# Kernel tuning notes

Hardware: AMD Instinct MI355X
Metric: run time of the kernel (lower is better)

Reference implementation:

```python
import jax, jax.numpy as jnp
import numpy as np

B, D = 8192, 768
TOP_K = 5


def setup_inputs() -> dict:
    key = jax.random.key(0)
    ks = jax.random.split(key, 12)
    # xavier_uniform bound for (D, D)
    bg = float(np.sqrt(6.0 / (D + D)))
    def xav(k, fan_in, fan_out):
        b = float(np.sqrt(6.0 / (fan_in + fan_out)))
        return jax.random.uniform(k, (fan_in, fan_out), jnp.float32, -b, b)
    return {
        "X": jax.random.normal(ks[0], (B, D), jnp.float32),
        "A_ecfp": jax.random.uniform(ks[1], (B, B), jnp.float32),
        "W_g": jax.random.uniform(ks[2], (D, D), jnp.float32, -bg, bg),
        "raw_alpha": jnp.zeros((), jnp.float32),
        "W_gcn": xav(ks[3], D, D),
        "b_gcn": jnp.zeros((D,), jnp.float32),
        "W1": xav(ks[4], D, 512),
        "b1": jnp.zeros((512,), jnp.float32),
        "W2": xav(ks[5], 512, 256),
        "b2": jnp.zeros((256,), jnp.float32),
        "W3": xav(ks[6], 256, 1),
        "b3": jnp.zeros((1,), jnp.float32),
    }


def _forward(X, A_ecfp, W_g, raw_alpha, W_gcn, b_gcn, W1, b1, W2, b2, W3, b3):
    n = X.shape[0]
    # learned similarity, blended with ECFP prior
    S = jax.nn.relu((X @ W_g) @ X.T)                    # (B, B)
    alpha = jax.nn.sigmoid(raw_alpha)
    A = alpha * A_ecfp + (1.0 - alpha) * S
    # top-k sparsification per row, symmetrized (OR)
    k = min(TOP_K, n - 1)
    _, top_idx = jax.lax.top_k(A, k)                    # (B, k)
    rows = jnp.arange(n)[:, None]
    mask = jnp.zeros_like(A).at[rows, top_idx].set(1.0)
    mask = ((mask + mask.T) > 0).astype(A.dtype)
    A = A * mask
    # zero diagonal, then add self-loops (diagonal becomes 1)
    diag = jnp.eye(n, dtype=A.dtype)
    A = A * (1.0 - diag) + diag
    # degree normalization D^-1 A
    D_inv = 1.0 / jnp.clip(A.sum(-1, keepdims=True), 1e-8)
    A_norm = A * D_inv
    # single GCN layer (exact erf GELU, matching torch default)
    H = jax.nn.gelu(A_norm @ X @ W_gcn + b_gcn, approximate=False)
    # MLP head (dropout is identity in eval)
    h = jax.nn.gelu(H @ W1 + b1, approximate=False)
    h = jax.nn.gelu(h @ W2 + b2, approximate=False)
    return h @ W3 + b3                                  # (B, 1)


def reference(X, A_ecfp, W_g, raw_alpha, W_gcn, b_gcn, W1, b1, W2, b2, W3, b3):
    return _forward(X, A_ecfp, W_g, raw_alpha, W_gcn, b_gcn, W1, b1, W2, b2, W3, b3)
```

## Files before the change

kernel.cpp:

```cpp
#include <hip/hip_runtime.h>
#include <math.h>


typedef __attribute__((ext_vector_type(8))) short short8v;
typedef __attribute__((ext_vector_type(4))) float f32x4;

__device__ __forceinline__ unsigned short f2bf(float f) {
  unsigned u = __float_as_uint(f);
  u += 0x7fffu + ((u >> 16) & 1u);
  return (unsigned short)(u >> 16);
}
__device__ __forceinline__ float bf2f(unsigned short h) {
  return __uint_as_float(((unsigned)h) << 16);
}
__device__ __forceinline__ float gelu_f(float x) {
  return 0.5f * x * (1.f + erff(x * 0.7071067811865475f));
}
__device__ __forceinline__ void gload16(const void* g, void* l) {
  __builtin_amdgcn_global_load_lds(
      (const __attribute__((address_space(1))) unsigned int*)g,
      (__attribute__((address_space(3))) unsigned int*)l, 16, 0, 0);
}

template <int N>
__device__ __forceinline__ void insN(float v, int j, float (&lv)[N], int (&li)[N]) {
#pragma unroll
  for (int p = N - 1; p >= 1; --p) {
    bool shiftv = v > lv[p - 1];
    bool here = (v > lv[p]) && !shiftv;
    float nv = shiftv ? lv[p - 1] : (here ? v : lv[p]);
    int ni = shiftv ? li[p - 1] : (here ? j : li[p]);
    lv[p] = nv; li[p] = ni;
  }
  if (v > lv[0]) { lv[0] = v; li[0] = j; }
}

__global__ __launch_bounds__(256) void cvt_bf16(const float* __restrict__ in,
                                                unsigned short* __restrict__ out, int n4) {
  int t = blockIdx.x * 256 + threadIdx.x;
  if (t >= n4) return;
  float4 f = ((const float4*)in)[t];
  ushort4 r;
  r.x = f2bf(f.x); r.y = f2bf(f.y); r.z = f2bf(f.z); r.w = f2bf(f.w);
  ((ushort4*)out)[t] = r;
}

__global__ __launch_bounds__(256) void split2(const float* __restrict__ in,
                                              unsigned short* __restrict__ out,
                                              int K, int n4) {
  int t = blockIdx.x * 256 + threadIdx.x;
  if (t >= n4) return;
  int kq = K >> 2;
  int row = t / kq, c4 = t - row * kq;
  float4 f = ((const float4*)in)[t];
  ushort4 h, l;
  float x;
  x = f.x; h.x = f2bf(x); l.x = f2bf(x - bf2f(h.x));
  x = f.y; h.y = f2bf(x); l.y = f2bf(x - bf2f(h.y));
  x = f.z; h.z = f2bf(x); l.z = f2bf(x - bf2f(h.z));
  x = f.w; h.w = f2bf(x); l.w = f2bf(x - bf2f(h.w));
  *(ushort4*)(out + (size_t)row * 2 * K + c4 * 4) = h;
  *(ushort4*)(out + (size_t)row * 2 * K + K + c4 * 4) = l;
}

__global__ __launch_bounds__(256) void split_wt2(const float* __restrict__ W,
                                                 unsigned short* __restrict__ t2,
                                                 int K, int N) {
  __shared__ float tile[32][33];
  int kb = blockIdx.x * 32, nb = blockIdx.y * 32;
  int tx = threadIdx.x & 31, ty = threadIdx.x >> 5;
#pragma unroll
  for (int p = 0; p < 4; ++p)
    tile[ty + p * 8][tx] = W[(size_t)(kb + ty + p * 8) * N + nb + tx];
  __syncthreads();
#pragma unroll
  for (int p = 0; p < 4; ++p) {
    int n = ty + p * 8;
    float x = tile[tx][n];
    unsigned short h = f2bf(x);
    unsigned short l = f2bf(x - bf2f(h));
    t2[(size_t)(nb + n) * (2 * K) + kb + tx] = h;
    t2[(size_t)(nb + n) * (2 * K) + K + kb + tx] = l;
  }
}

__global__ __launch_bounds__(256) void sgemm_f32(const float* __restrict__ A,
                                                 const float* __restrict__ Bm,
                                                 float* __restrict__ C,
                                                 unsigned short* __restrict__ Cbf,
                                                 int N, int K) {
  __shared__ float As[16][68];
  __shared__ float Bs[16][132];
  const int r0 = blockIdx.x * 64, c0 = blockIdx.y * 128;
  const int tid = threadIdx.x;
  const int tr = tid >> 4, tc = tid & 15;
  float acc[4][8];
#pragma unroll
  for (int i = 0; i < 4; ++i)
#pragma unroll
    for (int j = 0; j < 8; ++j) acc[i][j] = 0.f;

  for (int k0 = 0; k0 < K; k0 += 16) {
    {
      int row = tid >> 2, kq = tid & 3;
      float4 a4 = *(const float4*)(A + (size_t)(r0 + row) * K + k0 + kq * 4);
      As[kq * 4 + 0][row] = a4.x; As[kq * 4 + 1][row] = a4.y;
      As[kq * 4 + 2][row] = a4.z; As[kq * 4 + 3][row] = a4.w;
#pragma unroll
      for (int s = 0; s < 2; ++s) {
        int ch = tid + s * 256;
        int kk = ch >> 5, nq = ch & 31;
        *(float4*)&Bs[kk][nq * 4] = *(const float4*)(Bm + (size_t)(k0 + kk) * N + c0 + nq * 4);
      }
    }
    __syncthreads();
#pragma unroll
    for (int k = 0; k < 16; ++k) {
      float a[4], b[8];
      *(float4*)&a[0] = *(const float4*)&As[k][tr * 4];
      *(float4*)&b[0] = *(const float4*)&Bs[k][tc * 8];
      *(float4*)&b[4] = *(const float4*)&Bs[k][tc * 8 + 4];
#pragma unroll
      for (int i = 0; i < 4; ++i)
#pragma unroll
        for (int j = 0; j < 8; ++j) acc[i][j] = fmaf(a[i], b[j], acc[i][j]);
    }
    __syncthreads();
  }
#pragma unroll
  for (int i = 0; i < 4; ++i) {
    int r = r0 + tr * 4 + i;
#pragma unroll
    for (int jq = 0; jq < 2; ++jq) {
      *(float4*)(C + (size_t)r * N + c0 + tc * 8 + jq * 4) = *(float4*)&acc[i][jq * 4];
      ushort4 hb;
      hb.x = f2bf(acc[i][jq * 4 + 0]); hb.y = f2bf(acc[i][jq * 4 + 1]);
      hb.z = f2bf(acc[i][jq * 4 + 2]); hb.w = f2bf(acc[i][jq * 4 + 3]);
      *(ushort4*)(Cbf + (size_t)r * N + c0 + tc * 8 + jq * 4) = hb;
    }
  }
}

template <int EPI>
__global__ __launch_bounds__(256) void gemm_bt(const unsigned short* __restrict__ A,
                                               const unsigned short* __restrict__ Bt,
                                               const float* __restrict__ bias,
                                               float* __restrict__ C, int N, int K) {
  __shared__ __align__(16) unsigned short As[128 * 64];
  __shared__ __align__(16) unsigned short Bs[128 * 64];
  const int r0 = blockIdx.x * 128, c0 = blockIdx.y * 128;
  const int tid = threadIdx.x, lane = tid & 63, w = tid >> 6;
  const int wr = w >> 1, wc = w & 1;
  f32x4 acc[4][4];
  const f32x4 z4 = {0.f, 0.f, 0.f, 0.f};
#pragma unroll
  for (int i = 0; i < 4; ++i)
#pragma unroll
    for (int j = 0; j < 4; ++j) acc[i][j] = z4;

  const int srow = w * 32 + (lane >> 3);
  const int ksl = (lane & 7) ^ (lane >> 3);
  const unsigned short* aSrc = A + (size_t)(r0 + srow) * K + ksl * 8;
  const unsigned short* bSrc = Bt + (size_t)(c0 + srow) * K + ksl * 8;
  const int rsw = (lane & 7);

  for (int k0 = 0; k0 < K; k0 += 64) {
#pragma unroll
    for (int t = 0; t < 4; ++t) {
      gload16(aSrc + k0 + (size_t)t * 8 * K, (char*)As + (w * 32 + t * 8) * 128);
      gload16(bSrc + k0 + (size_t)t * 8 * K, (char*)Bs + (w * 32 + t * 8) * 128);
    }
    __syncthreads();
#pragma unroll
    for (int ks = 0; ks < 2; ++ks) {
      short8v af[4], bf[4];
      const int slot = ((ks * 4 + (lane >> 4)) ^ rsw) << 4;
#pragma unroll
      for (int f = 0; f < 4; ++f) {
        af[f] = *(const short8v*)((const char*)As + (wr * 64 + f * 16 + (lane & 15)) * 128 + slot);
        bf[f] = *(const short8v*)((const char*)Bs + (wc * 64 + f * 16 + (lane & 15)) * 128 + slot);
      }
#pragma unroll
      for (int fi = 0; fi < 4; ++fi)
#pragma unroll
        for (int fj = 0; fj < 4; ++fj)
          acc[fi][fj] = __builtin_amdgcn_mfma_f32_16x16x32_bf16(af[fi], bf[fj], acc[fi][fj], 0, 0, 0);
    }
    __syncthreads();
  }
#pragma unroll
  for (int fi = 0; fi < 4; ++fi)
#pragma unroll
    for (int fj = 0; fj < 4; ++fj) {
      int col = c0 + wc * 64 + fj * 16 + (lane & 15);
      int rowb = r0 + wr * 64 + fi * 16 + (lane >> 4) * 4;
#pragma unroll
      for (int r = 0; r < 4; ++r) {
        size_t idx = (size_t)(rowb + r) * N + col;
        float x = acc[fi][fj][r];
        if constexpr (EPI) x = gelu_f(x + bias[col]);
        C[idx] = x;
      }
    }
}

__global__ __launch_bounds__(512, 4) void s_topk(const unsigned short* __restrict__ Gh,
                                                 const unsigned short* __restrict__ Xh,
                                                 float* __restrict__ pv, int* __restrict__ pix) {
  __shared__ __align__(16) unsigned short As[128 * 64];
  __shared__ __align__(16) unsigned short Bs[128 * 64];
  const int bid = blockIdx.x;
  const int r0 = (bid >> 3) * 128;
  const int chunk = bid & 7;
  const int tid = threadIdx.x, lane = tid & 63, w = tid >> 6;
  const int wr = w >> 2, wc = w & 3;
  float lv0[5], lv1[5]; int li0[5], li1[5];
#pragma unroll
  for (int q = 0; q < 5; ++q) {
    lv0[q] = -1e30f; li0[q] = 0; lv1[q] = -1e30f; li1[q] = 0;
  }

  const int strow = tid >> 3, sslot = tid & 7;
  const int ksl = sslot ^ (strow & 7);
  const unsigned short* bSrc = Gh + (size_t)(r0 + strow) * 768 + ksl * 8;
  char* aDst0 = (char*)As + strow * 128 + sslot * 16;
  char* bDst0 = (char*)Bs + strow * 128 + sslot * 16;
  const int rsw = lane & 7;

  for (int jt = 0; jt < 8; ++jt) {
    const int j0 = chunk * 1024 + jt * 128;
    const unsigned short* aSrc = Xh + (size_t)(j0 + strow) * 768 + ksl * 8;
    f32x4 acc[4][2];
    const f32x4 z4 = {0.f, 0.f, 0.f, 0.f};
#pragma unroll
    for (int i = 0; i < 4; ++i) {
      acc[i][0] = z4; acc[i][1] = z4;
    }

    for (int k0 = 0; k0 < 768; k0 += 64) {
      gload16(aSrc + k0, aDst0);
      gload16(aSrc + k0 + (size_t)64 * 768, aDst0 + 64 * 128);
      gload16(bSrc + k0, bDst0);
      gload16(bSrc + k0 + (size_t)64 * 768, bDst0 + 64 * 128);
      __syncthreads();
#pragma unroll
      for (int ks = 0; ks < 2; ++ks) {
        short8v aj[4], bi[2];
        const int slot = ((ks * 4 + (lane >> 4)) ^ rsw) << 4;
#pragma unroll
        for (int f = 0; f < 4; ++f)
          aj[f] = *(const short8v*)((const char*)As + (wr * 64 + f * 16 + (lane & 15)) * 128 + slot);
#pragma unroll
        for (int f = 0; f < 2; ++f)
          bi[f] = *(const short8v*)((const char*)Bs + (wc * 32 + f * 16 + (lane & 15)) * 128 + slot);
#pragma unroll
        for (int fi = 0; fi < 4; ++fi) {
          acc[fi][0] = __builtin_amdgcn_mfma_f32_16x16x32_bf16(aj[fi], bi[0], acc[fi][0], 0, 0, 0);
          acc[fi][1] = __builtin_amdgcn_mfma_f32_16x16x32_bf16(aj[fi], bi[1], acc[fi][1], 0, 0, 0);
        }
      }
      __syncthreads();
    }
    const int jb = j0 + wr * 64 + (lane >> 4) * 4;
#pragma unroll
    for (int fi = 0; fi < 4; ++fi)
#pragma unroll
      for (int r = 0; r < 4; ++r) {
        int jj = jb + fi * 16 + r;
        float v0 = acc[fi][0][r];
        if (v0 > lv0[4]) insN<5>(v0, jj, lv0, li0);
        float v1 = acc[fi][1][r];
        if (v1 > lv1[4]) insN<5>(v1, jj, lv1, li1);
      }
  }
  const int slotw = wr * 4 + (lane >> 4);
  const int ib0 = r0 + wc * 32 + (lane & 15);
  size_t base0 = (((size_t)ib0 * 8 + chunk) * 8 + slotw) * 5;
#pragma unroll
  for (int q = 0; q < 5; ++q) { pv[base0 + q] = lv0[q]; pix[base0 + q] = li0[q]; }
  size_t base1 = (((size_t)(ib0 + 16) * 8 + chunk) * 8 + slotw) * 5;
#pragma unroll
  for (int q = 0; q < 5; ++q) { pv[base1 + q] = lv1[q]; pix[base1 + q] = li1[q]; }
}

__global__ __launch_bounds__(256) void merge16(const float* __restrict__ pv,
                                               const int* __restrict__ pix,
                                               int* __restrict__ gidx) {
  int row = blockIdx.x * 256 + threadIdx.x;
  float lv[16]; int li[16];
#pragma unroll
  for (int q = 0; q < 16; ++q) { lv[q] = -1e30f; li[q] = 0; }
  for (int ch = 0; ch < 8; ++ch)
#pragma unroll
    for (int sl = 0; sl < 8; ++sl) {
      size_t base = (((size_t)row * 8 + ch) * 8 + sl) * 5;
#pragma unroll
      for (int q = 0; q < 5; ++q) {
        float v = pv[base + q];
        if (v > lv[15]) insN<16>(v, pix[base + q], lv, li);
      }
    }
#pragma unroll
  for (int q = 0; q < 16; ++q) gidx[row * 16 + q] = li[q];
}

__global__ __launch_bounds__(256) void refine5(const float* __restrict__ G,
                                               const float* __restrict__ X,
                                               const float* __restrict__ Ae,
                                               const int* __restrict__ gidx,
                                               const float* __restrict__ ralpha,
                                               int* __restrict__ t5i, float* __restrict__ t5v) {
  int i = blockIdx.x * 4 + (threadIdx.x >> 6);
  int lane = threadIdx.x & 63;
  int c = lane >> 2, s = lane & 3;
  float sa = 1.f / (1.f + expf(-ralpha[0]));
  int j = gidx[i * 16 + c];
  const float* g = G + (size_t)i * 768;
  const float* x = X + (size_t)j * 768;
  float a = 0.f;
#pragma unroll 8
  for (int t = 0; t < 192; ++t) a = fmaf(g[s + 4 * t], x[s + 4 * t], a);
  a += __shfl_xor(a, 1);
  a += __shfl_xor(a, 2);
  float v = sa * Ae[(size_t)i * 8192 + j] + (1.f - sa) * fmaxf(a, 0.f);
  float vs[16]; int js[16];
#pragma unroll
  for (int q = 0; q < 16; ++q) { vs[q] = __shfl(v, q * 4); js[q] = __shfl(j, q * 4); }
  if (lane == 0) {
    unsigned used = 0;
#pragma unroll
    for (int t = 0; t < 5; ++t) {
      float bv = -1e30f; int bj = 0; int bq = 0; bool any = false;
#pragma unroll
      for (int q = 0; q < 16; ++q) {
        bool ok = ((used >> q) & 1u) == 0u;
        bool better = ok && (!any || vs[q] > bv || (vs[q] == bv && js[q] < bj));
        bv = better ? vs[q] : bv; bj = better ? js[q] : bj; bq = better ? q : bq;
        any = any || better;
      }
      used |= (1u << bq);
      t5v[(size_t)i * 5 + t] = bv;
      t5i[(size_t)i * 5 + t] = bj;
    }
  }
}

__global__ void edge_deg(const int* __restrict__ t5i, int* __restrict__ deg) {
  int e = blockIdx.x * 256 + threadIdx.x;
  if (e >= 40960) return;
  int i = e / 5, t = e - i * 5;
  int j = t5i[i * 5 + t];
  if (j == i) return;
  bool rev = false;
#pragma unroll
  for (int u = 0; u < 5; ++u) rev = rev || (t5i[j * 5 + u] == i);
  if (!rev || i < j) { atomicAdd(&deg[i], 1); atomicAdd(&deg[j], 1); }
}

__global__ void scan8k(const int* __restrict__ deg, int* __restrict__ off) {
  __shared__ int sums[256];
  int tid = threadIdx.x;
  int base = tid * 32;
  int s = 0;
  for (int u = 0; u < 32; ++u) s += deg[base + u];
  sums[tid] = s;
  __syncthreads();
  for (int d = 1; d < 256; d <<= 1) {
    int v = (tid >= d) ? sums[tid - d] : 0;
    __syncthreads();
    sums[tid] += v;
    __syncthreads();
  }
  int run = tid ? sums[tid - 1] : 0;
  for (int u = 0; u < 32; ++u) { off[base + u] = run; run += deg[base + u]; }
  if (tid == 255) off[8192] = run;
}

__global__ __launch_bounds__(256) void edge_fill(const int* __restrict__ t5i,
                                                 const float* __restrict__ t5v,
                                                 const float* __restrict__ G,
                                                 const float* __restrict__ X,
                                                 const float* __restrict__ Ae,
                                                 const float* __restrict__ ralpha,
                                                 const int* __restrict__ off,
                                                 int* __restrict__ cursor,
                                                 int* __restrict__ ccol, float* __restrict__ cval) {
  int e = blockIdx.x * 4 + (threadIdx.x >> 6);
  if (e >= 40960) return;
  int lane = threadIdx.x & 63;
  int i = e / 5, t = e - i * 5;
  int j = t5i[i * 5 + t];
  if (j == i) return;
  int rev = -1;
#pragma unroll
  for (int u = 0; u < 5; ++u)
    if (t5i[j * 5 + u] == i) rev = u;
  if (!(rev < 0 || i < j)) return;
  float vji;
  if (rev >= 0) {
    vji = t5v[j * 5 + rev];
  } else {
    const float* g = G + (size_t)j * 768;
    const float* x = X + (size_t)i * 768;
    float a = 0.f;
#pragma unroll
    for (int u = 0; u < 12; ++u) a = fmaf(g[lane + 64 * u], x[lane + 64 * u], a);
#pragma unroll
    for (int d = 32; d; d >>= 1) a += __shfl_xor(a, d);
    float sa = 1.f / (1.f + expf(-ralpha[0]));
    vji = sa * Ae[(size_t)j * 8192 + i] + (1.f - sa) * fmaxf(a, 0.f);
  }
  if (lane == 0) {
    float vij = t5v[i * 5 + t];
    int p0 = off[i] + atomicAdd(&cursor[i], 1);
    ccol[p0] = j; cval[p0] = vij;
    int p1 = off[j] + atomicAdd(&cursor[j], 1);
    ccol[p1] = i; cval[p1] = vji;
  }
}

__global__ __launch_bounds__(256) void gather_gcn(const float* __restrict__ X,
                                                  const int* __restrict__ off,
                                                  const int* __restrict__ ccol,
                                                  const float* __restrict__ cval,
                                                  float* __restrict__ M) {
  __shared__ float red[256];
  __shared__ float sdinv;
  int i = blockIdx.x, tid = threadIdx.x;
  int s0 = off[i], cnt = off[i + 1] - s0;
  float s = 0.f;
  for (int e = tid; e < cnt; e += 256) s += cval[s0 + e];
  red[tid] = s;
  __syncthreads();
  for (int d = 128; d; d >>= 1) {
    if (tid < d) red[tid] += red[tid + d];
    __syncthreads();
  }
  if (tid == 0) sdinv = 1.f / fmaxf(1.f + red[0], 1e-8f);
  __syncthreads();
  float dinv = sdinv;
  const float* xi = X + (size_t)i * 768;
  float a0 = xi[tid], a1 = xi[tid + 256], a2 = xi[tid + 512];
  for (int e = 0; e < cnt; ++e) {
    float v = cval[s0 + e];
    const float* xr = X + (size_t)ccol[s0 + e] * 768;
    a0 = fmaf(v, xr[tid], a0);
    a1 = fmaf(v, xr[tid + 256], a1);
    a2 = fmaf(v, xr[tid + 512], a2);
  }
  float* mi = M + (size_t)i * 768;
  mi[tid] = a0 * dinv; mi[tid + 256] = a1 * dinv; mi[tid + 512] = a2 * dinv;
}

__global__ __launch_bounds__(256) void final_head(const float* __restrict__ h2,
                                                  const float* __restrict__ W3,
                                                  const float* __restrict__ b3,
                                                  float* __restrict__ out) {
  int i = blockIdx.x * 4 + (threadIdx.x >> 6);
  int lane = threadIdx.x & 63;
  const float* r = h2 + (size_t)i * 256;
  float s = r[lane] * W3[lane] + r[lane + 64] * W3[lane + 64] +
            r[lane + 128] * W3[lane + 128] + r[lane + 192] * W3[lane + 192];
#pragma unroll
  for (int d = 32; d; d >>= 1) s += __shfl_xor(s, d);
  if (lane == 0) out[i] = s + b3[0];
}

extern "C" void kernel_launch(void* const* d_in, const int* in_sizes, int n_in,
                              void* d_out, int out_size, void* d_ws, size_t ws_size,
                              hipStream_t stream) {
  const float* X   = (const float*)d_in[0];
  const float* Ae  = (const float*)d_in[1];
  const float* Wg  = (const float*)d_in[2];
  const float* ra  = (const float*)d_in[3];
  const float* Wgc = (const float*)d_in[4];
  const float* bgc = (const float*)d_in[5];
  const float* W1  = (const float*)d_in[6];
  const float* b1  = (const float*)d_in[7];
  const float* W2  = (const float*)d_in[8];
  const float* b2  = (const float*)d_in[9];
  const float* W3  = (const float*)d_in[10];
  const float* b3  = (const float*)d_in[11];
  float* out = (float*)d_out;

  char* w = (char*)d_ws;
  size_t off_ = 0;
  auto take = [&](size_t n) -> void* {
    void* p = w + off_;
    off_ += (n + 255) & ~(size_t)255;
    return p;
  };
  float* G            = (float*)take((size_t)8192 * 768 * 4);
  unsigned short* Xh  = (unsigned short*)take((size_t)8192 * 768 * 2);
  unsigned short* Gh  = (unsigned short*)take((size_t)8192 * 768 * 2);
  float* pv           = (float*)take((size_t)8192 * 320 * 4);
  int* pix            = (int*)take((size_t)8192 * 320 * 4);
  int* gidx           = (int*)take((size_t)8192 * 16 * 4);
  int* t5i            = (int*)take((size_t)8192 * 5 * 4);
  float* t5v          = (float*)take((size_t)8192 * 5 * 4);
  int* deg            = (int*)take((size_t)8192 * 4);
  int* offr           = (int*)take((size_t)8193 * 4);
  int* cur            = (int*)take((size_t)8192 * 4);
  int* ccol           = (int*)take((size_t)81920 * 4);
  float* cval         = (float*)take((size_t)81920 * 4);
  unsigned short* Wc2 = (unsigned short*)take((size_t)768 * 1536 * 2);
  unsigned short* W12 = (unsigned short*)take((size_t)512 * 1536 * 2);
  unsigned short* W22 = (unsigned short*)take((size_t)256 * 1024 * 2);

  float* Mf  = (float*)Xh;
  float* Hf  = (float*)Xh;
  float* h1f = (float*)Xh;
  unsigned short* A2 = (unsigned short*)G;
  float* h2f = (float*)pv;

  sgemm_f32<<<dim3(128, 6), 256, 0, stream>>>(X, Wg, G, Gh, 768, 768);
  cvt_bf16<<<6144, 256, 0, stream>>>(X, Xh, 1572864);
  split_wt2<<<dim3(24, 24), 256, 0, stream>>>(Wgc, Wc2, 768, 768);
  split_wt2<<<dim3(24, 16), 256, 0, stream>>>(W1, W12, 768, 512);
  split_wt2<<<dim3(16, 8), 256, 0, stream>>>(W2, W22, 512, 256);

  s_topk<<<512, 512, 0, stream>>>(Gh, Xh, pv, pix);
  merge16<<<32, 256, 0, stream>>>(pv, pix, gidx);
  refine5<<<2048, 256, 0, stream>>>(G, X, Ae, gidx, ra, t5i, t5v);

  hipMemsetAsync(deg, 0, 8192 * 4, stream);
  hipMemsetAsync(cur, 0, 8192 * 4, stream);
  edge_deg<<<160, 256, 0, stream>>>(t5i, deg);
  scan8k<<<1, 256, 0, stream>>>(deg, offr);
  edge_fill<<<10240, 256, 0, stream>>>(t5i, t5v, G, X, Ae, ra, offr, cur, ccol, cval);

  gather_gcn<<<8192, 256, 0, stream>>>(X, offr, ccol, cval, Mf);

  split2<<<6144, 256, 0, stream>>>(Mf, A2, 768, 1572864);
  gemm_bt<1><<<dim3(64, 6), 256, 0, stream>>>(A2, Wc2, bgc, Hf, 768, 1536);

  split2<<<6144, 256, 0, stream>>>(Hf, A2, 768, 1572864);
  gemm_bt<1><<<dim3(64, 4), 256, 0, stream>>>(A2, W12, b1, h1f, 512, 1536);

  split2<<<4096, 256, 0, stream>>>(h1f, A2, 512, 1048576);
  gemm_bt<1><<<dim3(64, 2), 256, 0, stream>>>(A2, W22, b2, h2f, 256, 1024);

  final_head<<<2048, 256, 0, stream>>>(h2f, W3, b3, out);

  (void)in_sizes; (void)n_in; (void)out_size; (void)ws_size;
}
```

Measured before the change: 717.8 us.

## Fuse bf16 hi/lo split into GEMM epilogue and reorder s_topk block mapping

The GCN and first MLP GEMMs now emit GELU output directly as split bf16 hi/lo pairs, so the separate split2 conversion kernels and their fp32 round trip through memory are gone. The s_topk block index is remapped so that concurrently scheduled blocks cover a spread of row tiles and a shared column chunk, which is intended to change L2 reuse of the X chunks. The new epilogue writes scattered 2-byte stores, which may be less coalesced than the old float writes.

```diff
diff --git a/kernel.cpp b/kernel.cpp
--- a/kernel.cpp
+++ b/kernel.cpp
@@ -145,7 +145,9 @@
 __global__ __launch_bounds__(256) void gemm_bt(const unsigned short* __restrict__ A,
                                                const unsigned short* __restrict__ Bt,
                                                const float* __restrict__ bias,
-                                               float* __restrict__ C, int N, int K) {
+                                               float* __restrict__ C,
+                                               unsigned short* __restrict__ C2,
+                                               int N, int K) {
   __shared__ __align__(16) unsigned short As[128 * 64];
   __shared__ __align__(16) unsigned short Bs[128 * 64];
   const int r0 = blockIdx.x * 128, c0 = blockIdx.y * 128;
@@ -196,10 +198,18 @@
       int rowb = r0 + wr * 64 + fi * 16 + (lane >> 4) * 4;
 #pragma unroll
       for (int r = 0; r < 4; ++r) {
-        size_t idx = (size_t)(rowb + r) * N + col;
         float x = acc[fi][fj][r];
-        if constexpr (EPI) x = gelu_f(x + bias[col]);
-        C[idx] = x;
+        if constexpr (EPI == 0) {
+          C[(size_t)(rowb + r) * N + col] = x;
+        } else if constexpr (EPI == 1) {
+          C[(size_t)(rowb + r) * N + col] = gelu_f(x + bias[col]);
+        } else {
+          float y = gelu_f(x + bias[col]);
+          unsigned short h = f2bf(y);
+          unsigned short l = f2bf(y - bf2f(h));
+          C2[(size_t)(rowb + r) * 2 * N + col] = h;
+          C2[(size_t)(rowb + r) * 2 * N + N + col] = l;
+        }
       }
     }
 }
@@ -210,14 +220,15 @@
   __shared__ __align__(16) unsigned short As[128 * 64];
   __shared__ __align__(16) unsigned short Bs[128 * 64];
   const int bid = blockIdx.x;
-  const int r0 = (bid >> 3) * 128;
-  const int chunk = bid & 7;
+  const int p = bid & 7, q = bid >> 3;
+  const int r0 = (p * 8 + (q & 7)) * 128;
+  const int chunk = q >> 3;
   const int tid = threadIdx.x, lane = tid & 63, w = tid >> 6;
   const int wr = w >> 2, wc = w & 3;
   float lv0[5], lv1[5]; int li0[5], li1[5];
 #pragma unroll
-  for (int q = 0; q < 5; ++q) {
-    lv0[q] = -1e30f; li0[q] = 0; lv1[q] = -1e30f; li1[q] = 0;
+  for (int q2 = 0; q2 < 5; ++q2) {
+    lv0[q2] = -1e30f; li0[q2] = 0; lv1[q2] = -1e30f; li1[q2] = 0;
   }
 
   const int strow = tid >> 3, sslot = tid & 7;
@@ -277,10 +288,10 @@
   const int ib0 = r0 + wc * 32 + (lane & 15);
   size_t base0 = (((size_t)ib0 * 8 + chunk) * 8 + slotw) * 5;
 #pragma unroll
-  for (int q = 0; q < 5; ++q) { pv[base0 + q] = lv0[q]; pix[base0 + q] = li0[q]; }
+  for (int q2 = 0; q2 < 5; ++q2) { pv[base0 + q2] = lv0[q2]; pix[base0 + q2] = li0[q2]; }
   size_t base1 = (((size_t)(ib0 + 16) * 8 + chunk) * 8 + slotw) * 5;
 #pragma unroll
-  for (int q = 0; q < 5; ++q) { pv[base1 + q] = lv1[q]; pix[base1 + q] = li1[q]; }
+  for (int q2 = 0; q2 < 5; ++q2) { pv[base1 + q2] = lv1[q2]; pix[base1 + q2] = li1[q2]; }
 }
 
 __global__ __launch_bounds__(256) void merge16(const float* __restrict__ pv,
@@ -507,10 +518,10 @@
   unsigned short* W12 = (unsigned short*)take((size_t)512 * 1536 * 2);
   unsigned short* W22 = (unsigned short*)take((size_t)256 * 1024 * 2);
 
-  float* Mf  = (float*)Xh;
-  float* Hf  = (float*)Xh;
-  float* h1f = (float*)Xh;
-  unsigned short* A2 = (unsigned short*)G;
+  float* Mf            = (float*)Xh;
+  unsigned short* Hp2  = (unsigned short*)Xh;
+  unsigned short* A2   = (unsigned short*)G;
+  unsigned short* h1p2 = (unsigned short*)G;
   float* h2f = (float*)pv;
 
   sgemm_f32<<<dim3(128, 6), 256, 0, stream>>>(X, Wg, G, Gh, 768, 768);
@@ -532,13 +543,11 @@
   gather_gcn<<<8192, 256, 0, stream>>>(X, offr, ccol, cval, Mf);
 
   split2<<<6144, 256, 0, stream>>>(Mf, A2, 768, 1572864);
-  gemm_bt<1><<<dim3(64, 6), 256, 0, stream>>>(A2, Wc2, bgc, Hf, 768, 1536);
-
-  split2<<<6144, 256, 0, stream>>>(Hf, A2, 768, 1572864);
-  gemm_bt<1><<<dim3(64, 4), 256, 0, stream>>>(A2, W12, b1, h1f, 512, 1536);
-
-  split2<<<4096, 256, 0, stream>>>(h1f, A2, 512, 1048576);
-  gemm_bt<1><<<dim3(64, 2), 256, 0, stream>>>(A2, W22, b2, h2f, 256, 1024);
+  gemm_bt<2><<<dim3(64, 6), 256, 0, stream>>>(A2, Wc2, bgc, nullptr, Hp2, 768, 1536);
+
+  gemm_bt<2><<<dim3(64, 4), 256, 0, stream>>>(Hp2, W12, b1, nullptr, h1p2, 512, 1536);
+
+  gemm_bt<1><<<dim3(64, 2), 256, 0, stream>>>(h1p2, W22, b2, h2f, nullptr, 256, 1024);
 
   final_head<<<2048, 256, 0, stream>>>(h2f, W3, b3, out);
 
```

Result: faster. 683.7 us (-4.7%).
